# Optimization experiments

Hardware: AMD Instinct MI355X
Metric: run time of the kernel (lower is better)

The kernel has to match this reference:

```python
import math
import jax, jax.numpy as jnp
import numpy as np

B, S, D, H, DK, DV, L, DFF, V, NC, HID = 16, 512, 512, 8, 64, 64, 6, 2048, 32000, 5, 64


def setup_inputs() -> dict:
    key = jax.random.key(0)
    ks = jax.random.split(key, 32)
    def n(k, shape, scale=0.02):
        return jax.random.normal(k, shape, jnp.float32) * scale
    input_ids = jax.random.randint(ks[0], (B, S), 0, V).astype(jnp.int32)
    attention_mask = jnp.ones((B, S), jnp.bool_)
    emb = n(ks[1], (V, D)).at[0].set(0.0)  # padding_idx=0 row zeroed
    cls_token = jnp.zeros((D,), jnp.float32)
    return {
        "input_ids": input_ids,
        "attention_mask": attention_mask,
        "emb": emb,
        "cls_token": cls_token,
        "ln1_g": jnp.ones((L, D), jnp.float32), "ln1_b": jnp.zeros((L, D), jnp.float32),
        "ln2_g": jnp.ones((L, D), jnp.float32), "ln2_b": jnp.zeros((L, D), jnp.float32),
        "Wq": n(ks[2], (L, H, D, DK)), "bq": n(ks[3], (L, H, DK)),
        "Wk": n(ks[4], (L, H, D, DK)), "bk": n(ks[5], (L, H, DK)),
        "Wv": n(ks[6], (L, H, D, DV)), "bv": n(ks[7], (L, H, DV)),
        "Wo": n(ks[8], (L, H * DV, D)), "bo": n(ks[9], (L, D)),
        "W1": n(ks[10], (L, D, DFF)), "b1": n(ks[11], (L, DFF)),
        "W2": n(ks[12], (L, DFF, D)), "b2": n(ks[13], (L, D)),
        "Wc1": n(ks[14], (D, HID)), "bc1": n(ks[15], (HID,)),
        "Wc2": n(ks[16], (HID, NC)), "bc2": n(ks[17], (NC,)),
    }


def _layernorm(x, g, b, eps=1e-5):
    mu = jnp.mean(x, axis=-1, keepdims=True)
    var = jnp.var(x, axis=-1, keepdims=True)
    return (x - mu) * jax.lax.rsqrt(var + eps) * g + b


def _sinusoidal_pe(seq_len, d_model):
    pos = jnp.arange(seq_len, dtype=jnp.float32)[:, None]
    div = jnp.exp(jnp.arange(0, d_model, 2, dtype=jnp.float32) * (-math.log(10000.0) / d_model))
    pe = jnp.zeros((seq_len, d_model), jnp.float32)
    pe = pe.at[:, 0::2].set(jnp.sin(pos * div))
    pe = pe.at[:, 1::2].set(jnp.cos(pos * div))
    return pe


def _forward(input_ids, attention_mask, emb, cls_token,
             ln1_g, ln1_b, ln2_g, ln2_b,
             Wq, bq, Wk, bk, Wv, bv, Wo, bo,
             W1, b1, W2, b2, Wc1, bc1, Wc2, bc2):
    b, s = input_ids.shape
    x = emb[input_ids]                                     # [B,S,D]
    cls = jnp.broadcast_to(cls_token[None, None, :], (b, 1, x.shape[-1]))
    x = jnp.concatenate([cls, x], axis=1)                  # [B,S+1,D]
    full_mask = jnp.concatenate([jnp.ones((b, 1), jnp.bool_), attention_mask], axis=1)
    # pairwise attention mask [B, T, T]
    pair_mask = full_mask[:, None, :] & full_mask[:, :, None]
    x = x + _sinusoidal_pe(s + 1, x.shape[-1])[None]

    scale = 1.0 / math.sqrt(DK)

    def block(x, p):
        g1, be1, g2, be2, wq, bq_, wk, bk_, wv, bv_, wo, bo_, w1, bb1, w2, bb2 = p
        h = _layernorm(x, g1, be1)
        q = jnp.einsum('btd,hdk->bhtk', h, wq) + bq_[None, :, None, :]
        k = jnp.einsum('btd,hdk->bhtk', h, wk) + bk_[None, :, None, :]
        v = jnp.einsum('btd,hdv->bhtv', h, wv) + bv_[None, :, None, :]
        scores = jnp.einsum('bhqk,bhtk->bhqt', q, k) * scale
        scores = jnp.where(pair_mask[:, None, :, :], scores, -jnp.inf)
        attn = jax.nn.softmax(scores, axis=-1)
        o = jnp.einsum('bhqt,bhtv->bhqv', attn, v)          # [B,H,T,DV]
        o = o.transpose(0, 2, 1, 3).reshape(x.shape[0], x.shape[1], H * DV)
        x = x + o @ wo + bo_
        h2 = _layernorm(x, g2, be2)
        x = x + jnp.maximum(h2 @ w1 + bb1, 0.0) @ w2 + bb2
        return x, None

    params = (ln1_g, ln1_b, ln2_g, ln2_b, Wq, bq, Wk, bk, Wv, bv, Wo, bo, W1, b1, W2, b2)
    x, _ = jax.lax.scan(block, x, params)
    cls_out = x[:, 0]
    logits = jnp.maximum(cls_out @ Wc1 + bc1, 0.0) @ Wc2 + bc2
    return logits


def reference(input_ids, attention_mask, emb, cls_token,
              ln1_g, ln1_b, ln2_g, ln2_b,
              Wq, bq, Wk, bk, Wv, bv, Wo, bo,
              W1, b1, W2, b2, Wc1, bc1, Wc2, bc2):
    return _forward(input_ids, attention_mask, emb, cls_token,
                    ln1_g, ln1_b, ln2_g, ln2_b,
                    Wq, bq, Wk, bk, Wv, bv, Wo, bo,
                    W1, b1, W2, b2, Wc1, bc1, Wc2, bc2)
```

## Files before the change

kernel.cpp:

```cpp
#include <hip/hip_runtime.h>
#include <math.h>

#define DEV __device__ __forceinline__

typedef __attribute__((ext_vector_type(8))) short short8;
typedef __attribute__((ext_vector_type(4))) float f32x4;

DEV unsigned short f2bf(float f) {
  union { float f; unsigned int i; } v; v.f = f;
  unsigned int r = v.i + 0x7fffu + ((v.i >> 16) & 1u);
  return (unsigned short)(r >> 16);
}

DEV void lds16(const void* g, void* l) {
  __builtin_amdgcn_global_load_lds((__attribute__((address_space(1))) void*)(g),
                                   (__attribute__((address_space(3))) void*)(l), 16, 0, 0);
}


__global__ void transpose_g(const float* __restrict__ src, unsigned short* __restrict__ dst,
                            int Ksz, int Nsz) {
  __shared__ float tile[32][33];
  const int tx = threadIdx.x, ty = threadIdx.y;
  const int n0 = blockIdx.x * 32, k0 = blockIdx.y * 32;
  const size_t base = (size_t)blockIdx.z * Ksz * Nsz;
#pragma unroll
  for (int i = 0; i < 4; ++i)
    tile[ty + i * 8][tx] = src[base + (size_t)(k0 + ty + i * 8) * Nsz + n0 + tx];
  __syncthreads();
#pragma unroll
  for (int i = 0; i < 4; ++i)
    dst[base + (size_t)(n0 + ty + i * 8) * Ksz + k0 + tx] = f2bf(tile[tx][ty + i * 8]);
}

__global__ void pack_qkvT(const float* __restrict__ Wq, const float* __restrict__ Wk,
                          const float* __restrict__ Wv, unsigned short* __restrict__ dst) {
  __shared__ float tile[32][33];
  const int tx = threadIdx.x, ty = threadIdx.y;
  const int n0 = blockIdx.x * 32, k0 = blockIdx.y * 32, l = blockIdx.z;
  const int mat = n0 >> 9, hh = (n0 >> 6) & 7, dk0 = n0 & 63;
  const float* W = (mat == 0) ? Wq : (mat == 1) ? Wk : Wv;
  const float* Wl = W + ((size_t)l * 8 + hh) * 512 * 64;
#pragma unroll
  for (int i = 0; i < 4; ++i)
    tile[ty + i * 8][tx] = Wl[(size_t)(k0 + ty + i * 8) * 64 + dk0 + tx];
  __syncthreads();
#pragma unroll
  for (int i = 0; i < 4; ++i)
    dst[(size_t)l * 1536 * 512 + (size_t)(n0 + ty + i * 8) * 512 + k0 + tx] =
        f2bf(tile[tx][ty + i * 8]);
}

__global__ void pack_bias(const float* __restrict__ bq, const float* __restrict__ bk,
                          const float* __restrict__ bv, float* __restrict__ dst) {
  int i = blockIdx.x * 256 + threadIdx.x;
  if (i >= 6 * 1536) return;
  int l = i / 1536, c = i % 1536;
  float v = (c < 512) ? bq[l * 512 + c] : (c < 1024) ? bk[l * 512 + (c - 512)]
                                                     : bv[l * 512 + (c - 1024)];
  dst[i] = v;
}

__global__ void embed_kernel(const int* __restrict__ ids, const float* __restrict__ emb,
                             const float* __restrict__ cls, float* __restrict__ x) {
  int idx = blockIdx.x * 256 + threadIdx.x;
  int m = idx >> 9, d = idx & 511;
  int b = m / 513, t = m % 513;
  float v = (t == 0) ? cls[d] : emb[(size_t)ids[b * 512 + (t - 1)] * 512 + d];
  float fr = -(float)(d & ~1) * (9.2103403719761836f / 512.0f);
  float ang = (float)t * expf(fr);
  float pe = (d & 1) ? cosf(ang) : sinf(ang);
  x[idx] = v + pe;
}

template <int FUSE>
__global__ __launch_bounds__(256) void ln_kernel(float* __restrict__ x,
                                                 const float* __restrict__ g,
                                                 const float* __restrict__ bb,
                                                 unsigned short* __restrict__ h,
                                                 const float* __restrict__ part) {
  int wid = threadIdx.x >> 6, lane = threadIdx.x & 63;
  int m = blockIdx.x * 4 + wid;
  float* xr = x + (size_t)m * 512;
  float4 a = *(const float4*)(xr + lane * 8);
  float4 c = *(const float4*)(xr + lane * 8 + 4);
  if constexpr (FUSE) {
    const size_t PN = 8208ull * 512;
    const float* p = part + (size_t)m * 512 + lane * 8;
    float4 q0 = *(const float4*)(p),          q0b = *(const float4*)(p + 4);
    float4 q1 = *(const float4*)(p + PN),     q1b = *(const float4*)(p + PN + 4);
    float4 q2 = *(const float4*)(p + 2 * PN), q2b = *(const float4*)(p + 2 * PN + 4);
    a.x += q0.x + q1.x + q2.x;  a.y += q0.y + q1.y + q2.y;
    a.z += q0.z + q1.z + q2.z;  a.w += q0.w + q1.w + q2.w;
    c.x += q0b.x + q1b.x + q2b.x;  c.y += q0b.y + q1b.y + q2b.y;
    c.z += q0b.z + q1b.z + q2b.z;  c.w += q0b.w + q1b.w + q2b.w;
    *(float4*)(xr + lane * 8) = a;
    *(float4*)(xr + lane * 8 + 4) = c;
  }
  float s = a.x + a.y + a.z + a.w + c.x + c.y + c.z + c.w;
  float q = a.x * a.x + a.y * a.y + a.z * a.z + a.w * a.w +
            c.x * c.x + c.y * c.y + c.z * c.z + c.w * c.w;
#pragma unroll
  for (int d = 1; d < 64; d <<= 1) { s += __shfl_xor(s, d); q += __shfl_xor(q, d); }
  float mu = s * (1.f / 512.f);
  float var = q * (1.f / 512.f) - mu * mu;
  float rs = 1.f / sqrtf(var + 1e-5f);
  float4 g0 = *(const float4*)(g + lane * 8), g1 = *(const float4*)(g + lane * 8 + 4);
  float4 b0 = *(const float4*)(bb + lane * 8), b1 = *(const float4*)(bb + lane * 8 + 4);
  short8 ov;
  ov[0] = (short)f2bf((a.x - mu) * rs * g0.x + b0.x);
  ov[1] = (short)f2bf((a.y - mu) * rs * g0.y + b0.y);
  ov[2] = (short)f2bf((a.z - mu) * rs * g0.z + b0.z);
  ov[3] = (short)f2bf((a.w - mu) * rs * g0.w + b0.w);
  ov[4] = (short)f2bf((c.x - mu) * rs * g1.x + b1.x);
  ov[5] = (short)f2bf((c.y - mu) * rs * g1.y + b1.y);
  ov[6] = (short)f2bf((c.z - mu) * rs * g1.z + b1.z);
  ov[7] = (short)f2bf((c.w - mu) * rs * g1.w + b1.w);
  *(short8*)(h + (size_t)m * 512 + lane * 8) = ov;
}

template <int EPI>
DEV void gemm_epilogue(f32x4 (&acc)[4][4], const float* __restrict__ bias,
                       unsigned short* __restrict__ Cbf, float* __restrict__ Cres,
                       unsigned short* __restrict__ vT, float* __restrict__ part,
                       int M, int N, int m0, int n0, int wm, int wn, int l15, int l4,
                       int bz) {
  const bool z0 = (bz == 0);
  const size_t MN = (size_t)M * N;
#pragma unroll
  for (int i = 0; i < 4; ++i) {
#pragma unroll
    for (int j = 0; j < 4; ++j) {
      const int gn = n0 + wn + j * 16 + l15;
      float bv = bias[gn];
      if constexpr (EPI == 2) {
        if (!z0) bv = 0.f;
      }
#pragma unroll
      for (int r = 0; r < 4; ++r) {
        const int gm = m0 + wm + i * 16 + l4 * 4 + r;
        if (gm < M) {
          float v = acc[i][j][r] + bv;
          if constexpr (EPI == 1) v = fmaxf(v, 0.f);
          if constexpr (EPI == 2) {
            if (z0) {
              Cres[(size_t)gm * N + gn] += v;
            } else {
              part[(size_t)(bz - 1) * MN + (size_t)gm * N + gn] = v;
            }
          } else if constexpr (EPI == 3) {
            if (gn < 1024) {
              Cbf[(size_t)gm * N + gn] = f2bf(v);
            } else {
              int b = gm / 513, t = gm - b * 513;
              vT[(size_t)(b * 512 + (gn - 1024)) * 528 + t] = f2bf(v);
            }
          } else {
            Cbf[(size_t)gm * N + gn] = f2bf(v);
          }
        }
      }
    }
  }
}

template <int EPI>
__global__ __launch_bounds__(256) void gemm_bt(const unsigned short* __restrict__ A,
                                               const unsigned short* __restrict__ Bt,
                                               const float* __restrict__ bias,
                                               unsigned short* __restrict__ Cbf,
                                               float* __restrict__ Cres,
                                               unsigned short* __restrict__ vT,
                                               float* __restrict__ part,
                                               int M, int N, int K, int lda) {
  __shared__ __align__(16) unsigned short As[2][128 * 64];
  __shared__ __align__(16) unsigned short Bs[2][128 * 64];
  const int tid = threadIdx.x, w = tid >> 6, lane = tid & 63;
  const int l15 = lane & 15, l4 = lane >> 4;
  const int gx = gridDim.x;
  const int nwg = gx * gridDim.y;
  const int id = blockIdx.y * gx + blockIdx.x;
  const int xcd = id & 7, orig = id >> 3;
  const int qq = nwg >> 3, rr = nwg & 7;
  const int newid = (xcd < rr ? xcd * (qq + 1) : rr * (qq + 1) + (xcd - rr) * qq) + orig;
  const int m0 = (newid % gx) * 128, n0 = (newid / gx) * 128;
  const int wm = (w >> 1) * 64, wn = (w & 1) * 64;
  const int kbase = blockIdx.z * K;
  f32x4 acc[4][4] = {};
  const int nk = K >> 6;
  auto stage = [&](int buf, int kt) {
#pragma unroll
    for (int r = 0; r < 4; ++r) {
      int s = r * 4 + w;
      int ol = s * 1024 + lane * 16;
      int ra = ol >> 7, cp = (ol >> 4) & 7;
      int co = ((cp ^ (ra & 7)) * 8) + kt * 64;
      lds16(A + (size_t)(m0 + ra) * lda + kbase + co, (char*)As[buf] + s * 1024);
      lds16(Bt + (size_t)(n0 + ra) * lda + kbase + co, (char*)Bs[buf] + s * 1024);
    }
  };
  stage(0, 0);
  __syncthreads();
  int cur = 0;
  for (int kt = 0; kt < nk; ++kt) {
    if (kt + 1 < nk) stage(cur ^ 1, kt + 1);
#pragma unroll
    for (int kk = 0; kk < 2; ++kk) {
      short8 af[4], bfr[4];
#pragma unroll
      for (int i = 0; i < 4; ++i) {
        int ar = wm + i * 16 + l15;
        af[i] = *(const short8*)&As[cur][ar * 64 + (((kk * 4 + l4) ^ (ar & 7)) * 8)];
        int br = wn + i * 16 + l15;
        bfr[i] = *(const short8*)&Bs[cur][br * 64 + (((kk * 4 + l4) ^ (br & 7)) * 8)];
      }
#pragma unroll
      for (int i = 0; i < 4; ++i)
#pragma unroll
        for (int j = 0; j < 4; ++j)
          acc[i][j] = __builtin_amdgcn_mfma_f32_16x16x32_bf16(af[i], bfr[j], acc[i][j], 0, 0, 0);
    }
    __syncthreads();
    cur ^= 1;
  }
  gemm_epilogue<EPI>(acc, bias, Cbf, Cres, vT, part, M, N, m0, n0, wm, wn, l15, l4,
                     blockIdx.z);
}

template <int EPI>
__global__ __launch_bounds__(512) void gemm_wide(const unsigned short* __restrict__ A,
                                                 const unsigned short* __restrict__ Bt,
                                                 const float* __restrict__ bias,
                                                 unsigned short* __restrict__ Cbf,
                                                 float* __restrict__ Cres,
                                                 unsigned short* __restrict__ vT,
                                                 float* __restrict__ part,
                                                 int M, int N, int K, int lda) {
  __shared__ __align__(16) unsigned short As[2][128 * 64];
  __shared__ __align__(16) unsigned short Bs[2][256 * 64];
  const int tid = threadIdx.x, w = tid >> 6, lane = tid & 63;
  const int l15 = lane & 15, l4 = lane >> 4;
  const int gx = gridDim.x;
  const int nwg = gx * gridDim.y;
  const int id = blockIdx.y * gx + blockIdx.x;
  const int xcd = id & 7, orig = id >> 3;
  const int qq = nwg >> 3, rr = nwg & 7;
  const int newid = (xcd < rr ? xcd * (qq + 1) : rr * (qq + 1) + (xcd - rr) * qq) + orig;
  const int m0 = (newid % gx) * 128, n0 = (newid / gx) * 256;
  const int wm = (w >> 2) * 64, wn = (w & 3) * 64;
  const int kbase = blockIdx.z * K;
  f32x4 acc[4][4] = {};
  const int nk = K >> 6;
  auto stage = [&](int buf, int kt) {
#pragma unroll
    for (int r = 0; r < 2; ++r) {
      int s = r * 8 + w;
      int ol = s * 1024 + lane * 16;
      int ra = ol >> 7, cp = (ol >> 4) & 7;
      int co = ((cp ^ (ra & 7)) * 8) + kt * 64;
      lds16(A + (size_t)(m0 + ra) * lda + kbase + co, (char*)As[buf] + s * 1024);
    }
#pragma unroll
    for (int r = 0; r < 4; ++r) {
      int s = r * 8 + w;
      int ol = s * 1024 + lane * 16;
      int rb = ol >> 7, cp = (ol >> 4) & 7;
      int co = ((cp ^ (rb & 7)) * 8) + kt * 64;
      lds16(Bt + (size_t)(n0 + rb) * lda + kbase + co, (char*)Bs[buf] + s * 1024);
    }
  };
  stage(0, 0);
  __syncthreads();
  int cur = 0;
  for (int kt = 0; kt < nk; ++kt) {
    if (kt + 1 < nk) stage(cur ^ 1, kt + 1);
#pragma unroll
    for (int kk = 0; kk < 2; ++kk) {
      short8 af[4], bfr[4];
#pragma unroll
      for (int i = 0; i < 4; ++i) {
        int ar = wm + i * 16 + l15;
        af[i] = *(const short8*)&As[cur][ar * 64 + (((kk * 4 + l4) ^ (ar & 7)) * 8)];
        int br = wn + i * 16 + l15;
        bfr[i] = *(const short8*)&Bs[cur][br * 64 + (((kk * 4 + l4) ^ (br & 7)) * 8)];
      }
#pragma unroll
      for (int i = 0; i < 4; ++i)
#pragma unroll
        for (int j = 0; j < 4; ++j)
          acc[i][j] = __builtin_amdgcn_mfma_f32_16x16x32_bf16(af[i], bfr[j], acc[i][j], 0, 0, 0);
    }
    __syncthreads();
    cur ^= 1;
  }
  gemm_epilogue<EPI>(acc, bias, Cbf, Cres, vT, part, M, N, m0, n0, wm, wn, l15, l4,
                     blockIdx.z);
}

__global__ __launch_bounds__(256) void reduce3(const float* __restrict__ p,
                                               float* __restrict__ x) {
  const size_t PN = 8208ull * 512;
  size_t i = ((size_t)blockIdx.x * 256 + threadIdx.x) * 4;
  float4 a = *(const float4*)(x + i);
  float4 b0 = *(const float4*)(p + i);
  float4 b1 = *(const float4*)(p + PN + i);
  float4 b2 = *(const float4*)(p + 2 * PN + i);
  a.x += b0.x + b1.x + b2.x;
  a.y += b0.y + b1.y + b2.y;
  a.z += b0.z + b1.z + b2.z;
  a.w += b0.w + b1.w + b2.w;
  *(float4*)(x + i) = a;
}

__global__ __launch_bounds__(256) void attn_kernel(const unsigned short* __restrict__ qkv,
                                                   const unsigned short* __restrict__ vT,
                                                   unsigned short* __restrict__ o) {
  const int qt = blockIdx.x, bh = blockIdx.y;
  const int b = bh >> 3, hh = bh & 7;
  const int tid = threadIdx.x, w = tid >> 6, lane = tid & 63;
  const int l15 = lane & 15, l4 = lane >> 4;
  __shared__ __align__(16) unsigned short Ks[2][64 * 64];
  __shared__ __align__(16) unsigned short Vs[2][64 * 64];
  __shared__ __align__(16) unsigned short Ps[64 * 72];
  const int q0 = qt * 64;
  const size_t qbase = (size_t)b * 513 * 1536;
  short8 qf[2];
  {
    const unsigned short* qp =
        qkv + qbase + (size_t)(q0 + w * 16 + l15) * 1536 + hh * 64 + l4 * 8;
    qf[0] = *(const short8*)qp;
    qf[1] = *(const short8*)(qp + 32);
  }
  f32x4 oacc[4] = {};
  float lpart[4] = {};
  auto stage = [&](int buf, int kvt) {
    const int kv0 = kvt * 64;
#pragma unroll
    for (int r = 0; r < 2; ++r) {
      int ol = (r * 4 + w) * 1024 + lane * 16;
      int rk = ol >> 7, cp = (ol >> 4) & 7;
      int sw = (cp ^ (rk & 7)) * 8;
      lds16(qkv + qbase + (size_t)(kv0 + rk) * 1536 + 512 + hh * 64 + sw,
            (char*)Ks[buf] + ol);
      lds16(vT + (size_t)(bh * 64 + rk) * 528 + kv0 + sw, (char*)Vs[buf] + ol);
    }
  };
  stage(0, 0);
  __syncthreads();
  int cur = 0;
  for (int kvt = 0; kvt < 9; ++kvt) {
    const int kv0 = kvt * 64;
    if (kvt + 1 < 9) stage(cur ^ 1, kvt + 1);
    f32x4 sacc[4] = {};
#pragma unroll
    for (int kk = 0; kk < 2; ++kk)
#pragma unroll
      for (int nf = 0; nf < 4; ++nf) {
        int kr = nf * 16 + l15;
        short8 kf = *(const short8*)&Ks[cur][kr * 64 + (((kk * 4 + l4) ^ (kr & 7)) * 8)];
        sacc[nf] = __builtin_amdgcn_mfma_f32_16x16x32_bf16(qf[kk], kf, sacc[nf], 0, 0, 0);
      }
#pragma unroll
    for (int nf = 0; nf < 4; ++nf) {
      const bool valid = (kv0 + nf * 16 + l15) < 513;
#pragma unroll
      for (int r = 0; r < 4; ++r) {
        float p = valid ? __expf(sacc[nf][r] * 0.125f) : 0.f;
        lpart[r] += p;
        Ps[(w * 16 + l4 * 4 + r) * 72 + nf * 16 + l15] = f2bf(p);
      }
    }
#pragma unroll
    for (int kk = 0; kk < 2; ++kk) {
      short8 pa = *(const short8*)&Ps[(w * 16 + l15) * 72 + kk * 32 + l4 * 8];
#pragma unroll
      for (int nf = 0; nf < 4; ++nf) {
        int dvr = nf * 16 + l15;
        short8 vf = *(const short8*)&Vs[cur][dvr * 64 + (((kk * 4 + l4) ^ (dvr & 7)) * 8)];
        oacc[nf] = __builtin_amdgcn_mfma_f32_16x16x32_bf16(pa, vf, oacc[nf], 0, 0, 0);
      }
    }
    __syncthreads();
    cur ^= 1;
  }
#pragma unroll
  for (int d = 1; d < 16; d <<= 1)
#pragma unroll
    for (int r = 0; r < 4; ++r) lpart[r] += __shfl_xor(lpart[r], d);
#pragma unroll
  for (int nf = 0; nf < 4; ++nf)
#pragma unroll
    for (int r = 0; r < 4; ++r) {
      int q = q0 + w * 16 + l4 * 4 + r;
      if (q < 513) {
        float val = oacc[nf][r] / lpart[r];
        o[((size_t)b * 513 + q) * 512 + hh * 64 + nf * 16 + l15] = f2bf(val);
      }
    }
}

__global__ void cls_kernel(const float* __restrict__ x, const float* __restrict__ Wc1,
                           const float* __restrict__ bc1, const float* __restrict__ Wc2,
                           const float* __restrict__ bc2, float* __restrict__ out) {
  int b = blockIdx.x, j = threadIdx.x;
  const float* xr = x + (size_t)b * 513 * 512;
  float acc = bc1[j];
  for (int d = 0; d < 512; ++d) acc += xr[d] * Wc1[d * 64 + j];
  acc = fmaxf(acc, 0.f);
  __shared__ float hid[64];
  hid[j] = acc;
  __syncthreads();
  if (j < 5) {
    float lg = bc2[j];
#pragma unroll
    for (int d2 = 0; d2 < 64; ++d2) lg += hid[d2] * Wc2[d2 * 5 + j];
    out[b * 5 + j] = lg;
  }
}

extern "C" void kernel_launch(void* const* d_in, const int* in_sizes, int n_in,
                              void* d_out, int out_size, void* d_ws, size_t ws_size,
                              hipStream_t stream) {
  const int* ids = (const int*)d_in[0];
  const float* emb = (const float*)d_in[2];
  const float* cls = (const float*)d_in[3];
  const float* ln1g = (const float*)d_in[4];
  const float* ln1b = (const float*)d_in[5];
  const float* ln2g = (const float*)d_in[6];
  const float* ln2b = (const float*)d_in[7];
  const float* Wq = (const float*)d_in[8];
  const float* bq = (const float*)d_in[9];
  const float* Wk = (const float*)d_in[10];
  const float* bk = (const float*)d_in[11];
  const float* Wv = (const float*)d_in[12];
  const float* bv = (const float*)d_in[13];
  const float* Wo = (const float*)d_in[14];
  const float* bo = (const float*)d_in[15];
  const float* W1 = (const float*)d_in[16];
  const float* b1 = (const float*)d_in[17];
  const float* W2 = (const float*)d_in[18];
  const float* b2 = (const float*)d_in[19];
  const float* Wc1 = (const float*)d_in[20];
  const float* bc1 = (const float*)d_in[21];
  const float* Wc2 = (const float*)d_in[22];
  const float* bc2 = (const float*)d_in[23];

  char* ws = (char*)d_ws;
  size_t off = 0;
  auto alloc = [&](size_t bytes) {
    char* p = ws + off;
    off += (bytes + 255) & ~(size_t)255;
    return p;
  };
  const size_t QKV_ELEMS = 8320ull * 1536;
  const size_t VT_ELEMS = 16ull * 512 * 528 + 528;
  const size_t FFN_ELEMS = 8320ull * 2048;
  const size_t BIGU = (QKV_ELEMS + VT_ELEMS > FFN_ELEMS) ? QKV_ELEMS + VT_ELEMS : FFN_ELEMS;

  unsigned short* wqkvT = (unsigned short*)alloc(6ull * 1536 * 512 * 2);
  unsigned short* woT = (unsigned short*)alloc(6ull * 512 * 512 * 2);
  unsigned short* w1T = (unsigned short*)alloc(6ull * 2048 * 512 * 2);
  unsigned short* w2T = (unsigned short*)alloc(6ull * 512 * 2048 * 2);
  float* bqkv = (float*)alloc(6ull * 1536 * 4);
  float* x = (float*)alloc(8208ull * 512 * 4);
  unsigned short* hbuf = (unsigned short*)alloc(8320ull * 512 * 2);
  unsigned short* obuf = (unsigned short*)alloc(8320ull * 512 * 2);
  unsigned short* big = (unsigned short*)alloc(BIGU * 2);
  float* fpart = (float*)alloc(3ull * 8208 * 512 * 4);
  unsigned short* vT = big + QKV_ELEMS;
  if (off > ws_size) return;

  hipMemsetAsync(hbuf + 8208ull * 512, 0, 112ull * 512 * 2, stream);
  hipMemsetAsync(obuf + 8208ull * 512, 0, 112ull * 512 * 2, stream);
  hipMemsetAsync(big + 8208ull * 1536, 0, 112ull * 1536 * 2, stream);
  hipMemsetAsync(vT, 0, VT_ELEMS * 2, stream);

  pack_qkvT<<<dim3(48, 16, 6), dim3(32, 8), 0, stream>>>(Wq, Wk, Wv, wqkvT);
  transpose_g<<<dim3(16, 16, 6), dim3(32, 8), 0, stream>>>(Wo, woT, 512, 512);
  transpose_g<<<dim3(64, 16, 6), dim3(32, 8), 0, stream>>>(W1, w1T, 512, 2048);
  transpose_g<<<dim3(16, 64, 6), dim3(32, 8), 0, stream>>>(W2, w2T, 2048, 512);
  pack_bias<<<36, 256, 0, stream>>>(bq, bk, bv, bqkv);
  embed_kernel<<<16416, 256, 0, stream>>>(ids, emb, cls, x);

  for (int l = 0; l < 6; ++l) {
    if (l == 0)
      ln_kernel<0><<<2052, 256, 0, stream>>>(x, ln1g + l * 512, ln1b + l * 512, hbuf,
                                             nullptr);
    else
      ln_kernel<1><<<2052, 256, 0, stream>>>(x, ln1g + l * 512, ln1b + l * 512, hbuf,
                                             fpart);
    gemm_wide<3><<<dim3(65, 6), 512, 0, stream>>>(hbuf, wqkvT + (size_t)l * 1536 * 512,
                                                  bqkv + l * 1536, big, nullptr, vT,
                                                  nullptr, 8208, 1536, 512, 512);
    attn_kernel<<<dim3(9, 128), 256, 0, stream>>>(big, vT, obuf);
    gemm_bt<2><<<dim3(65, 4), 256, 0, stream>>>(obuf, woT + (size_t)l * 512 * 512,
                                                bo + l * 512, nullptr, x, nullptr,
                                                nullptr, 8208, 512, 512, 512);
    ln_kernel<0><<<2052, 256, 0, stream>>>(x, ln2g + l * 512, ln2b + l * 512, hbuf,
                                           nullptr);
    gemm_wide<1><<<dim3(65, 8), 512, 0, stream>>>(hbuf, w1T + (size_t)l * 2048 * 512,
                                                  b1 + l * 2048, big, nullptr, nullptr,
                                                  nullptr, 8208, 2048, 512, 512);
    gemm_wide<2><<<dim3(65, 2, 4), 512, 0, stream>>>(big, w2T + (size_t)l * 512 * 2048,
                                                     b2 + l * 512, nullptr, x, nullptr,
                                                     fpart, 8208, 512, 512, 2048);
  }
  reduce3<<<4104, 256, 0, stream>>>(fpart, x);
  cls_kernel<<<16, 64, 0, stream>>>(x, Wc1, bc1, Wc2, bc2, (float*)d_out);
}
```

Baseline: 1.492 ms.

## Halve GEMM K-tile and use explicit partial vmcnt waits with raw barriers

Both GEMM kernels now stage 32-wide K tiles instead of 64, with a 4-way XOR swizzle in place of the 8-way one, which halves their LDS footprint. Every `__syncthreads` in the GEMM and attention loops becomes a raw `s_barrier` plus explicit `s_waitcnt vmcnt(N)`. That waits only for the current buffer's direct-to-LDS loads and leaves the prefetch of the next tile in flight. The aim is better overlap of global loads with MFMA work and possibly higher occupancy, at the cost of twice as many loop iterations and barriers per GEMM and less MFMA work between syncs. The hand-counted vmcnt values depend on the exact number of loads issued per stage.

After: 1.410 ms. 1.06x faster.

```diff
diff --git a/kernel.cpp b/kernel.cpp
--- a/kernel.cpp
+++ b/kernel.cpp
@@ -5,6 +5,12 @@
 
 typedef __attribute__((ext_vector_type(8))) short short8;
 typedef __attribute__((ext_vector_type(4))) float f32x4;
+
+#define BAR() __builtin_amdgcn_s_barrier()
+#define FENCE() asm volatile("" ::: "memory")
+#define WAIT_VM0() asm volatile("s_waitcnt vmcnt(0)" ::: "memory")
+#define WAIT_VM3() asm volatile("s_waitcnt vmcnt(3)" ::: "memory")
+#define WAIT_VM4() asm volatile("s_waitcnt vmcnt(4)" ::: "memory")
 
 DEV unsigned short f2bf(float f) {
   union { float f; unsigned int i; } v; v.f = f;
@@ -173,8 +179,8 @@
                                                unsigned short* __restrict__ vT,
                                                float* __restrict__ part,
                                                int M, int N, int K, int lda) {
-  __shared__ __align__(16) unsigned short As[2][128 * 64];
-  __shared__ __align__(16) unsigned short Bs[2][128 * 64];
+  __shared__ __align__(16) unsigned short As[2][128 * 32];
+  __shared__ __align__(16) unsigned short Bs[2][128 * 32];
   const int tid = threadIdx.x, w = tid >> 6, lane = tid & 63;
   const int l15 = lane & 15, l4 = lane >> 4;
   const int gx = gridDim.x;
@@ -187,40 +193,42 @@
   const int wm = (w >> 1) * 64, wn = (w & 1) * 64;
   const int kbase = blockIdx.z * K;
   f32x4 acc[4][4] = {};
-  const int nk = K >> 6;
+  const int nk = K >> 5;
   auto stage = [&](int buf, int kt) {
 #pragma unroll
-    for (int r = 0; r < 4; ++r) {
+    for (int r = 0; r < 2; ++r) {
       int s = r * 4 + w;
       int ol = s * 1024 + lane * 16;
-      int ra = ol >> 7, cp = (ol >> 4) & 7;
-      int co = ((cp ^ (ra & 7)) * 8) + kt * 64;
-      lds16(A + (size_t)(m0 + ra) * lda + kbase + co, (char*)As[buf] + s * 1024);
-      lds16(Bt + (size_t)(n0 + ra) * lda + kbase + co, (char*)Bs[buf] + s * 1024);
+      int ra = ol >> 6, cp = (ol >> 4) & 3;
+      int co = ((cp ^ (ra & 3)) * 8) + kt * 32;
+      lds16(A + (size_t)(m0 + ra) * lda + kbase + co, (char*)As[buf] + ol);
+      lds16(Bt + (size_t)(n0 + ra) * lda + kbase + co, (char*)Bs[buf] + ol);
     }
   };
   stage(0, 0);
-  __syncthreads();
+  WAIT_VM0();
+  BAR();
+  FENCE();
   int cur = 0;
   for (int kt = 0; kt < nk; ++kt) {
-    if (kt + 1 < nk) stage(cur ^ 1, kt + 1);
-#pragma unroll
-    for (int kk = 0; kk < 2; ++kk) {
-      short8 af[4], bfr[4];
-#pragma unroll
-      for (int i = 0; i < 4; ++i) {
-        int ar = wm + i * 16 + l15;
-        af[i] = *(const short8*)&As[cur][ar * 64 + (((kk * 4 + l4) ^ (ar & 7)) * 8)];
-        int br = wn + i * 16 + l15;
-        bfr[i] = *(const short8*)&Bs[cur][br * 64 + (((kk * 4 + l4) ^ (br & 7)) * 8)];
-      }
-#pragma unroll
-      for (int i = 0; i < 4; ++i)
-#pragma unroll
-        for (int j = 0; j < 4; ++j)
-          acc[i][j] = __builtin_amdgcn_mfma_f32_16x16x32_bf16(af[i], bfr[j], acc[i][j], 0, 0, 0);
-    }
-    __syncthreads();
+    if (kt + 1 < nk) { stage(cur ^ 1, kt + 1); WAIT_VM4(); } else { WAIT_VM0(); }
+    BAR();
+    FENCE();
+    short8 af[4], bfr[4];
+#pragma unroll
+    for (int i = 0; i < 4; ++i) {
+      int ar = wm + i * 16 + l15;
+      af[i] = *(const short8*)&As[cur][ar * 32 + ((l4 ^ (ar & 3)) * 8)];
+      int br = wn + i * 16 + l15;
+      bfr[i] = *(const short8*)&Bs[cur][br * 32 + ((l4 ^ (br & 3)) * 8)];
+    }
+#pragma unroll
+    for (int i = 0; i < 4; ++i)
+#pragma unroll
+      for (int j = 0; j < 4; ++j)
+        acc[i][j] = __builtin_amdgcn_mfma_f32_16x16x32_bf16(af[i], bfr[j], acc[i][j], 0, 0, 0);
+    FENCE();
+    BAR();
     cur ^= 1;
   }
   gemm_epilogue<EPI>(acc, bias, Cbf, Cres, vT, part, M, N, m0, n0, wm, wn, l15, l4,
@@ -236,8 +244,8 @@
                                                  unsigned short* __restrict__ vT,
                                                  float* __restrict__ part,
                                                  int M, int N, int K, int lda) {
-  __shared__ __align__(16) unsigned short As[2][128 * 64];
-  __shared__ __align__(16) unsigned short Bs[2][256 * 64];
+  __shared__ __align__(16) unsigned short As[2][128 * 32];
+  __shared__ __align__(16) unsigned short Bs[2][256 * 32];
   const int tid = threadIdx.x, w = tid >> 6, lane = tid & 63;
   const int l15 = lane & 15, l4 = lane >> 4;
   const int gx = gridDim.x;
@@ -250,47 +258,48 @@
   const int wm = (w >> 2) * 64, wn = (w & 3) * 64;
   const int kbase = blockIdx.z * K;
   f32x4 acc[4][4] = {};
-  const int nk = K >> 6;
+  const int nk = K >> 5;
   auto stage = [&](int buf, int kt) {
+    {
+      int s = w;
+      int ol = s * 1024 + lane * 16;
+      int ra = ol >> 6, cp = (ol >> 4) & 3;
+      int co = ((cp ^ (ra & 3)) * 8) + kt * 32;
+      lds16(A + (size_t)(m0 + ra) * lda + kbase + co, (char*)As[buf] + ol);
+    }
 #pragma unroll
     for (int r = 0; r < 2; ++r) {
       int s = r * 8 + w;
       int ol = s * 1024 + lane * 16;
-      int ra = ol >> 7, cp = (ol >> 4) & 7;
-      int co = ((cp ^ (ra & 7)) * 8) + kt * 64;
-      lds16(A + (size_t)(m0 + ra) * lda + kbase + co, (char*)As[buf] + s * 1024);
-    }
-#pragma unroll
-    for (int r = 0; r < 4; ++r) {
-      int s = r * 8 + w;
-      int ol = s * 1024 + lane * 16;
-      int rb = ol >> 7, cp = (ol >> 4) & 7;
-      int co = ((cp ^ (rb & 7)) * 8) + kt * 64;
-      lds16(Bt + (size_t)(n0 + rb) * lda + kbase + co, (char*)Bs[buf] + s * 1024);
+      int rb = ol >> 6, cp = (ol >> 4) & 3;
+      int co = ((cp ^ (rb & 3)) * 8) + kt * 32;
+      lds16(Bt + (size_t)(n0 + rb) * lda + kbase + co, (char*)Bs[buf] + ol);
     }
   };
   stage(0, 0);
-  __syncthreads();
+  WAIT_VM0();
+  BAR();
+  FENCE();
   int cur = 0;
   for (int kt = 0; kt < nk; ++kt) {
-    if (kt + 1 < nk) stage(cur ^ 1, kt + 1);
-#pragma unroll
-    for (int kk = 0; kk < 2; ++kk) {
-      short8 af[4], bfr[4];
-#pragma unroll
-      for (int i = 0; i < 4; ++i) {
-        int ar = wm + i * 16 + l15;
-        af[i] = *(const short8*)&As[cur][ar * 64 + (((kk * 4 + l4) ^ (ar & 7)) * 8)];
-        int br = wn + i * 16 + l15;
-        bfr[i] = *(const short8*)&Bs[cur][br * 64 + (((kk * 4 + l4) ^ (br & 7)) * 8)];
-      }
-#pragma unroll
-      for (int i = 0; i < 4; ++i)
-#pragma unroll
-        for (int j = 0; j < 4; ++j)
-          acc[i][j] = __builtin_amdgcn_mfma_f32_16x16x32_bf16(af[i], bfr[j], acc[i][j], 0, 0, 0);
-    }
-    __syncthreads();
+    if (kt + 1 < nk) { stage(cur ^ 1, kt + 1); WAIT_VM3(); } else { WAIT_VM0(); }
+    BAR();
+    FENCE();
+    short8 af[4], bfr[4];
+#pragma unroll
+    for (int i = 0; i < 4; ++i) {
+      int ar = wm + i * 16 + l15;
+      af[i] = *(const short8*)&As[cur][ar * 32 + ((l4 ^ (ar & 3)) * 8)];
+      int br = wn + i * 16 + l15;
+      bfr[i] = *(const short8*)&Bs[cur][br * 32 + ((l4 ^ (br & 3)) * 8)];
+    }
+#pragma unroll
+    for (int i = 0; i < 4; ++i)
+#pragma unroll
+      for (int j = 0; j < 4; ++j)
+        acc[i][j] = __builtin_amdgcn_mfma_f32_16x16x32_bf16(af[i], bfr[j], acc[i][j], 0, 0, 0);
+    FENCE();
+    BAR();
     cur ^= 1;
   }
   gemm_epilogue<EPI>(acc, bias, Cbf, Cres, vT, part, M, N, m0, n0, wm, wn, l15, l4,
@@ -346,11 +355,15 @@
     }
   };
   stage(0, 0);
-  __syncthreads();
+  WAIT_VM0();
+  BAR();
+  FENCE();
   int cur = 0;
   for (int kvt = 0; kvt < 9; ++kvt) {
     const int kv0 = kvt * 64;
-    if (kvt + 1 < 9) stage(cur ^ 1, kvt + 1);
+    if (kvt + 1 < 9) { stage(cur ^ 1, kvt + 1); WAIT_VM4(); } else { WAIT_VM0(); }
+    BAR();
+    FENCE();
     f32x4 sacc[4] = {};
 #pragma unroll
     for (int kk = 0; kk < 2; ++kk)
@@ -380,7 +393,8 @@
         oacc[nf] = __builtin_amdgcn_mfma_f32_16x16x32_bf16(pa, vf, oacc[nf], 0, 0, 0);
       }
     }
-    __syncthreads();
+    FENCE();
+    BAR();
     cur ^= 1;
   }
 #pragma unroll
```
